# Kernel tuning notes

Measured on AMD Instinct MI355X. Metric: run time of the kernel, lower is better.

## Reference

```python
import jax, jax.numpy as jnp
import numpy as np

GROUPS = 8
EPS = 1e-5


def setup_inputs() -> dict:
    key = jax.random.key(0)
    ks = jax.random.split(key, 3)
    b, c, h, w = 8, 256, 64, 64
    return {
        "x": jax.random.normal(ks[0], (b, c, h, w), dtype=jnp.float32),
        "norm_w": jnp.ones((c,), jnp.float32),
        "norm_b": jnp.zeros((c,), jnp.float32),
        "qkv_w": jax.random.normal(ks[1], (3 * c, c), dtype=jnp.float32) * (1.0 / np.sqrt(c)),
        "qkv_b": jnp.zeros((3 * c,), jnp.float32),
        "proj_w": jax.random.normal(ks[2], (c, c), dtype=jnp.float32) * (1.0 / np.sqrt(c)),
        "proj_b": jnp.zeros((c,), jnp.float32),
    }


def _group_norm(x, w, b):
    B, C, H, W = x.shape
    xg = x.reshape(B, GROUPS, C // GROUPS, H, W)
    mean = xg.mean(axis=(2, 3, 4), keepdims=True)
    var = xg.var(axis=(2, 3, 4), keepdims=True)
    xn = ((xg - mean) * jax.lax.rsqrt(var + EPS)).reshape(B, C, H, W)
    return xn * w[None, :, None, None] + b[None, :, None, None]


def reference(x, norm_w, norm_b, qkv_w, qkv_b, proj_w, proj_b):
    B, C, H, W = x.shape
    xn = _group_norm(x, norm_w, norm_b)
    # 1x1 conv == per-pixel matmul: [B,3C,H,W]
    qkv = jnp.einsum('bchw,oc->bohw', xn, qkv_w) + qkv_b[None, :, None, None]
    q, k, v = jnp.split(qkv, 3, axis=1)  # each [B,C,H,W]
    hw = H * W
    q = q.reshape(B, C, hw).transpose(0, 2, 1)  # [B,hw,C]
    k = k.reshape(B, C, hw)                     # [B,C,hw]
    v = v.reshape(B, C, hw).transpose(0, 2, 1)  # [B,hw,C]
    scores = jnp.einsum('bnc,bcm->bnm', q, k) / jnp.sqrt(jnp.asarray(C, x.dtype))
    attn = jax.nn.softmax(scores, axis=-1)      # [B,hw,hw]
    out = jnp.einsum('bnm,bmc->bnc', attn, v)   # [B,hw,C]
    out = out.transpose(0, 2, 1).reshape(B, C, H, W)
    out = jnp.einsum('bchw,oc->bohw', out, proj_w) + proj_b[None, :, None, None]
    return x + out
```

## Files before the change

### kernel.cpp

```cpp
#include <hip/hip_runtime.h>
#include <stdint.h>

#define BATCH 8
#define CH 256
#define HW 4096
#define OC 768

typedef __bf16 bf16;
typedef __attribute__((ext_vector_type(8))) __bf16 bf16x8;
typedef __attribute__((ext_vector_type(4))) __bf16 bf16x4;
typedef __attribute__((ext_vector_type(4))) float f32x4;
typedef long fp8x8;

#define MFMA16(a, b, c) __builtin_amdgcn_mfma_f32_16x16x32_bf16(a, b, c, 0, 0, 0)
#define MFMA8(a, b, c) __builtin_amdgcn_mfma_f32_16x16x32_fp8_fp8(a, b, c, 0, 0, 0)
#define LOG2E 1.44269504088896f

static __device__ __forceinline__ void gl2lds16(const void* g, void* l) {
  __builtin_amdgcn_global_load_lds((const __attribute__((address_space(1))) void*)g,
                                   (__attribute__((address_space(3))) void*)l, 16, 0, 0);
}

static __device__ __forceinline__ int pack4fp8(float a, float b, float c, float d) {
  int t = __builtin_amdgcn_cvt_pk_fp8_f32(a, b, 0, false);
  return __builtin_amdgcn_cvt_pk_fp8_f32(c, d, t, true);
}

__global__ __launch_bounds__(256) void trans_stats(const float* __restrict__ x,
    bf16* __restrict__ xt, float* __restrict__ partial) {
  __shared__ float tile[32][33];
  __shared__ float red[8];
  int b = blockIdx.z, ct = blockIdx.y, pt = blockIdx.x;
  int p0 = pt * 32, c0 = ct * 32;
  const float* xb = x + (size_t)b * CH * HW;
  float s = 0.f, s2 = 0.f;
#pragma unroll
  for (int i = 0; i < 4; i++) {
    int c = c0 + threadIdx.y + i * 8;
    float v = xb[(size_t)c * HW + p0 + threadIdx.x];
    tile[threadIdx.y + i * 8][threadIdx.x] = v;
    s += v;
    s2 += v * v;
  }
  int tid = threadIdx.y * 32 + threadIdx.x;
  for (int off = 32; off; off >>= 1) { s += __shfl_down(s, off); s2 += __shfl_down(s2, off); }
  if ((tid & 63) == 0) { red[(tid >> 6) * 2] = s; red[(tid >> 6) * 2 + 1] = s2; }
  __syncthreads();
  if (tid == 0) {
    float* pp = partial + ((size_t)(b * 8 + ct) * 128 + pt) * 2;
    pp[0] = red[0] + red[2] + red[4] + red[6];
    pp[1] = red[1] + red[3] + red[5] + red[7];
  }
  bf16* xtb = xt + (size_t)b * HW * CH;
#pragma unroll
  for (int i = 0; i < 4; i++) {
    int p = p0 + threadIdx.y + i * 8;
    xtb[(size_t)p * CH + c0 + threadIdx.x] = (bf16)tile[threadIdx.x][threadIdx.y + i * 8];
  }
}

__global__ __launch_bounds__(128) void gn_finalize(const float* __restrict__ partial,
    const float* __restrict__ nw, const float* __restrict__ nb,
    float* __restrict__ scale, float* __restrict__ shift) {
  int bg = blockIdx.x;
  int t = threadIdx.x;
  const float* pp = partial + (size_t)bg * 128 * 2;
  float s = pp[t * 2], s2 = pp[t * 2 + 1];
  __shared__ float red[4], mm[2];
  for (int off = 32; off; off >>= 1) { s += __shfl_down(s, off); s2 += __shfl_down(s2, off); }
  if ((t & 63) == 0) { red[(t >> 6) * 2] = s; red[(t >> 6) * 2 + 1] = s2; }
  __syncthreads();
  if (t == 0) {
    float ts = red[0] + red[2], ts2 = red[1] + red[3];
    float mean = ts * (1.0f / 131072.0f);
    float var = ts2 * (1.0f / 131072.0f) - mean * mean;
    mm[0] = mean;
    mm[1] = rsqrtf(var + 1e-5f);
  }
  __syncthreads();
  if (t < 32) {
    int b = bg >> 3, g = bg & 7, c = g * 32 + t;
    float sc = nw[c] * mm[1];
    scale[b * CH + c] = sc;
    shift[b * CH + c] = nb[c] - mm[0] * sc;
  }
}

__global__ __launch_bounds__(256) void fold_qkv(const float* __restrict__ qkv_w,
    const float* __restrict__ qkv_b, const float* __restrict__ scale,
    const float* __restrict__ shift, bf16* __restrict__ wq, float* __restrict__ bq) {
  int o = blockIdx.x, b = blockIdx.y, c = threadIdx.x;
  float w = qkv_w[o * CH + c];
  wq[((size_t)b * OC + o) * CH + c] = (bf16)(w * scale[b * CH + c]);
  float part = w * shift[b * CH + c];
  __shared__ float red[4];
  for (int off = 32; off; off >>= 1) part += __shfl_down(part, off);
  if ((threadIdx.x & 63) == 0) red[threadIdx.x >> 6] = part;
  __syncthreads();
  if (threadIdx.x == 0) bq[b * OC + o] = qkv_b[o] + red[0] + red[1] + red[2] + red[3];
}

__global__ __launch_bounds__(256) void conv_projw(const float* __restrict__ w,
                                                  bf16* __restrict__ wb) {
  int i = blockIdx.x * 256 + threadIdx.x;
  wb[i] = (bf16)w[i];
}

__global__ __launch_bounds__(256) void qkv_gemm(const bf16* __restrict__ wq,
    const float* __restrict__ bq, const bf16* __restrict__ xt,
    uint8_t* __restrict__ qt, uint8_t* __restrict__ kt, uint8_t* __restrict__ vv) {
  __shared__ __align__(16) bf16 As[2][128 * 32];
  __shared__ __align__(16) bf16 Bs[2][128 * 32];
  int b = blockIdx.z, row0 = blockIdx.y * 128, col0 = blockIdx.x * 128;
  const bf16* A = wq + (size_t)b * OC * CH + (size_t)row0 * CH;
  const bf16* Bt = xt + (size_t)b * HW * CH + (size_t)col0 * CH;
  int tid = threadIdx.x, lane = tid & 63, wave = tid >> 6;
  int wm = (wave & 1) * 64, wn = (wave >> 1) * 64;
  int l15 = lane & 15, quad = lane >> 4;
  auto stage = [&](int buf, int k0) {
#pragma unroll
    for (int i = 0; i < 2; i++) {
      int idx = i * 256 + tid, r = idx >> 2, ch = idx & 3;
      gl2lds16(A + (size_t)r * CH + k0 + ch * 8, &As[buf][idx * 8]);
    }
#pragma unroll
    for (int i = 0; i < 2; i++) {
      int idx = i * 256 + tid, r = idx >> 2, ch = idx & 3;
      gl2lds16(Bt + (size_t)r * CH + k0 + ch * 8, &Bs[buf][idx * 8]);
    }
  };
  f32x4 zero = {0.f, 0.f, 0.f, 0.f};
  f32x4 acc[4][4];
#pragma unroll
  for (int i = 0; i < 4; i++)
#pragma unroll
    for (int j = 0; j < 4; j++) acc[i][j] = zero;
  stage(0, 0);
  for (int kk = 0; kk < 8; kk++) {
    int cur = kk & 1;
    __syncthreads();
    if (kk < 7) stage(1 - cur, (kk + 1) * 32);
    bf16x8 af[4], bfr[4];
#pragma unroll
    for (int i = 0; i < 4; i++) {
      af[i] = *(const bf16x8*)(&As[cur][(wm + i * 16 + l15) * 32 + quad * 8]);
      bfr[i] = *(const bf16x8*)(&Bs[cur][(wn + i * 16 + l15) * 32 + quad * 8]);
    }
#pragma unroll
    for (int i = 0; i < 4; i++)
#pragma unroll
      for (int j = 0; j < 4; j++) acc[i][j] = MFMA16(af[i], bfr[j], acc[i][j]);
  }
#pragma unroll
  for (int i = 0; i < 4; i++) {
    int o = row0 + wm + i * 16 + quad * 4;
#pragma unroll
    for (int j = 0; j < 4; j++) {
      int p = col0 + wn + j * 16 + l15;
      float v[4];
#pragma unroll
      for (int r = 0; r < 4; r++) v[r] = acc[i][j][r] + bq[b * OC + o + r];
      if (o < CH) {
        *(int*)(qt + ((size_t)b * HW + p) * CH + o) =
            pack4fp8(v[0] * LOG2E, v[1] * LOG2E, v[2] * LOG2E, v[3] * LOG2E);
      } else if (o < 2 * CH) {
        *(int*)(kt + ((size_t)b * HW + p) * CH + (o - CH)) = pack4fp8(v[0], v[1], v[2], v[3]);
      } else {
#pragma unroll
        for (int r = 0; r < 4; r++) {
          int t8 = __builtin_amdgcn_cvt_pk_fp8_f32(v[r], 0.f, 0, false);
          vv[((size_t)b * CH + (o - 2 * CH + r)) * HW + p] = (uint8_t)(t8 & 0xff);
        }
      }
    }
  }
}

__global__ __launch_bounds__(256, 2) void attn(const uint8_t* __restrict__ qt,
    const uint8_t* __restrict__ kt, const uint8_t* __restrict__ vv,
    bf16* __restrict__ opart, float* __restrict__ lstat) {
  __shared__ __align__(16) uint8_t Ks[2][32 * 256];
  __shared__ __align__(16) uint8_t Vs[2][256 * 32];
  int b = blockIdx.z, mh = blockIdx.y, q0 = blockIdx.x * 128;
  int tid = threadIdx.x, lane = tid & 63, w = tid >> 6;
  int l15 = lane & 15, quad = lane >> 4;
  int q1 = quad >> 1, qh = quad & 1;
  const uint8_t* kb_base = kt + (size_t)b * HW * CH;
  const uint8_t* vb_base = vv + (size_t)b * CH * HW;
  auto stageKV = [&](int buf, int m0) {
    const uint8_t* kb = kb_base + (size_t)m0 * CH;
#pragma unroll
    for (int i = 0; i < 2; i++) {
      int idx = i * 256 + tid, m = idx >> 4, p16 = idx & 15;
      gl2lds16(kb + m * CH + (p16 ^ (m & 7)) * 16, &Ks[buf][idx * 16]);
    }
#pragma unroll
    for (int i = 0; i < 2; i++) {
      int idx = i * 256 + tid, c = idx >> 1;
      int h2 = (idx & 1) ^ ((idx >> 3) & 1);
      gl2lds16(vb_base + (size_t)c * HW + m0 + h2 * 16, &Vs[buf][idx * 16]);
    }
  };
  fp8x8 qf[2][8];
  const uint8_t* qb = qt + ((size_t)b * HW + q0 + w * 32) * CH;
#pragma unroll
  for (int ns = 0; ns < 2; ns++)
#pragma unroll
    for (int kc = 0; kc < 8; kc++)
      qf[ns][kc] = *(const fp8x8*)(qb + (size_t)(ns * 16 + l15) * CH + kc * 32 + quad * 8);
  f32x4 zero = {0.f, 0.f, 0.f, 0.f};
  f32x4 o[2][16];
#pragma unroll
  for (int ns = 0; ns < 2; ns++)
#pragma unroll
    for (int t = 0; t < 16; t++) o[ns][t] = zero;
  float lsum[2] = {0.f, 0.f};
  int kswz = l15 & 7;
  int vswz = (l15 >> 2) & 1;
  stageKV(0, mh * 2048);
  for (int mt = 0; mt < 64; mt++) {
    int cur = mt & 1;
    __syncthreads();
    if (mt < 63) stageKV(1 - cur, mh * 2048 + (mt + 1) * 32);
    f32x4 s[2][2];
#pragma unroll
    for (int ms = 0; ms < 2; ms++)
#pragma unroll
      for (int ns = 0; ns < 2; ns++) s[ms][ns] = zero;
#pragma unroll
    for (int kc = 0; kc < 8; kc++) {
      fp8x8 kf[2];
#pragma unroll
      for (int ms = 0; ms < 2; ms++)
        kf[ms] = *(const fp8x8*)(&Ks[cur][(ms * 16 + l15) * 256 +
                                          (((kc * 2 + q1) ^ kswz) * 16) + qh * 8]);
#pragma unroll
      for (int ms = 0; ms < 2; ms++)
#pragma unroll
        for (int ns = 0; ns < 2; ns++) s[ms][ns] = MFMA8(kf[ms], qf[ns][kc], s[ms][ns]);
    }
    fp8x8 pa[2];
#pragma unroll
    for (int ns = 0; ns < 2; ns++) {
      float p0[4], p1[4];
#pragma unroll
      for (int r = 0; r < 4; r++) {
        p0[r] = exp2f(fmaf(s[0][ns][r], 0.0625f, -2.0f));
        lsum[ns] += p0[r];
      }
#pragma unroll
      for (int r = 0; r < 4; r++) {
        p1[r] = exp2f(fmaf(s[1][ns][r], 0.0625f, -2.0f));
        lsum[ns] += p1[r];
      }
      int pk0 = pack4fp8(p0[0], p0[1], p0[2], p0[3]);
      int pk1 = pack4fp8(p1[0], p1[1], p1[2], p1[3]);
      int srcLo = ((quad & 1) * 32 + l15) << 2;
      int srcHi = srcLo + 64;
      int a0 = __builtin_amdgcn_ds_bpermute(srcLo, pk0);
      int a1 = __builtin_amdgcn_ds_bpermute(srcLo, pk1);
      int b0 = __builtin_amdgcn_ds_bpermute(srcHi, pk0);
      int b1 = __builtin_amdgcn_ds_bpermute(srcHi, pk1);
      int2 pr;
      pr.x = q1 ? a1 : a0;
      pr.y = q1 ? b1 : b0;
      pa[ns] = __builtin_bit_cast(long, pr);
    }
#pragma unroll
    for (int t = 0; t < 16; t++) {
      fp8x8 vf = *(const fp8x8*)(&Vs[cur][(2 * (t * 16 + l15) + (q1 ^ vswz)) * 16 + qh * 8]);
      o[0][t] = MFMA8(vf, pa[0], o[0][t]);
      o[1][t] = MFMA8(vf, pa[1], o[1][t]);
    }
  }
  int ncol = q0 + w * 32 + l15;
#pragma unroll
  for (int ns = 0; ns < 2; ns++) {
    float lt = lsum[ns];
    lt += __shfl_xor(lt, 16);
    lt += __shfl_xor(lt, 32);
    float inv = 1.0f / lt;
    bf16* ob = opart + (size_t)(mh * BATCH + b) * CH * HW + ncol + ns * 16;
#pragma unroll
    for (int t = 0; t < 16; t++)
#pragma unroll
      for (int r = 0; r < 4; r++)
        ob[(size_t)(t * 16 + quad * 4 + r) * HW] = (bf16)(o[ns][t][r] * inv);
    if (quad == 0)
      lstat[(size_t)(mh * BATCH + b) * HW + ncol + ns * 16] = lt;
  }
}

__global__ __launch_bounds__(256) void combine_t(const bf16* __restrict__ opart,
    const float* __restrict__ lstat, bf16* __restrict__ ot) {
  __shared__ float tile[32][33];
  int b = blockIdx.z, p0 = blockIdx.x * 32, c0 = blockIdx.y * 32;
  int tx = threadIdx.x, ty = threadIdx.y;
  int p = p0 + tx;
  float l0 = lstat[(size_t)(0 * BATCH + b) * HW + p];
  float l1 = lstat[(size_t)(1 * BATCH + b) * HW + p];
  float inv = 1.0f / (l0 + l1);
  float w0 = l0 * inv, w1 = l1 * inv;
#pragma unroll
  for (int i = 0; i < 4; i++) {
    int c = c0 + ty + i * 8;
    tile[ty + i * 8][tx] =
        w0 * (float)opart[((size_t)(0 * BATCH + b) * CH + c) * HW + p] +
        w1 * (float)opart[((size_t)(1 * BATCH + b) * CH + c) * HW + p];
  }
  __syncthreads();
#pragma unroll
  for (int i = 0; i < 4; i++) {
    int pp = p0 + ty + i * 8;
    ot[((size_t)b * HW + pp) * CH + c0 + tx] = (bf16)tile[tx][ty + i * 8];
  }
}

__global__ __launch_bounds__(256) void proj_gemm(const bf16* __restrict__ pw,
    const float* __restrict__ pbias, const bf16* __restrict__ ot,
    const float* __restrict__ x, float* __restrict__ out) {
  __shared__ __align__(16) bf16 As[2][128 * 32];
  __shared__ __align__(16) bf16 Bs[2][128 * 32];
  int b = blockIdx.z, row0 = blockIdx.y * 128, col0 = blockIdx.x * 128;
  const bf16* A = pw + (size_t)row0 * CH;
  const bf16* Bt = ot + (size_t)b * HW * CH + (size_t)col0 * CH;
  int tid = threadIdx.x, lane = tid & 63, wave = tid >> 6;
  int wm = (wave & 1) * 64, wn = (wave >> 1) * 64;
  int l15 = lane & 15, quad = lane >> 4;
  auto stage = [&](int buf, int k0) {
#pragma unroll
    for (int i = 0; i < 2; i++) {
      int idx = i * 256 + tid, r = idx >> 2, ch = idx & 3;
      gl2lds16(A + (size_t)r * CH + k0 + ch * 8, &As[buf][idx * 8]);
    }
#pragma unroll
    for (int i = 0; i < 2; i++) {
      int idx = i * 256 + tid, r = idx >> 2, ch = idx & 3;
      gl2lds16(Bt + (size_t)r * CH + k0 + ch * 8, &Bs[buf][idx * 8]);
    }
  };
  f32x4 zero = {0.f, 0.f, 0.f, 0.f};
  f32x4 acc[4][4];
#pragma unroll
  for (int i = 0; i < 4; i++)
#pragma unroll
    for (int j = 0; j < 4; j++) acc[i][j] = zero;
  stage(0, 0);
  for (int kk = 0; kk < 8; kk++) {
    int cur = kk & 1;
    __syncthreads();
    if (kk < 7) stage(1 - cur, (kk + 1) * 32);
    bf16x8 af[4], bfr[4];
#pragma unroll
    for (int i = 0; i < 4; i++) {
      af[i] = *(const bf16x8*)(&As[cur][(wm + i * 16 + l15) * 32 + quad * 8]);
      bfr[i] = *(const bf16x8*)(&Bs[cur][(wn + i * 16 + l15) * 32 + quad * 8]);
    }
#pragma unroll
    for (int i = 0; i < 4; i++)
#pragma unroll
      for (int j = 0; j < 4; j++) acc[i][j] = MFMA16(af[i], bfr[j], acc[i][j]);
  }
#pragma unroll
  for (int i = 0; i < 4; i++) {
#pragma unroll
    for (int j = 0; j < 4; j++) {
      int p = col0 + wn + j * 16 + l15;
#pragma unroll
      for (int r = 0; r < 4; r++) {
        int oo = row0 + wm + i * 16 + quad * 4 + r;
        size_t off = ((size_t)b * CH + oo) * HW + p;
        out[off] = x[off] + pbias[oo] + acc[i][j][r];
      }
    }
  }
}

extern "C" void kernel_launch(void* const* d_in, const int* in_sizes, int n_in,
                              void* d_out, int out_size, void* d_ws, size_t ws_size,
                              hipStream_t stream) {
  const float* x = (const float*)d_in[0];
  const float* nw = (const float*)d_in[1];
  const float* nb = (const float*)d_in[2];
  const float* qkvw = (const float*)d_in[3];
  const float* qkvb = (const float*)d_in[4];
  const float* projw = (const float*)d_in[5];
  const float* projb = (const float*)d_in[6];
  float* out = (float*)d_out;
  char* ws = (char*)d_ws;
  float* scale = (float*)(ws + 0);
  float* shift = (float*)(ws + 8192);
  float* bq    = (float*)(ws + 16384);
  bf16* pwb    = (bf16*)(ws + 40960);
  bf16* wq     = (bf16*)(ws + 172032);
  bf16* xt     = (bf16*)(ws + 3317760);
  uint8_t* qt  = (uint8_t*)(ws + 20094976);
  uint8_t* kt  = (uint8_t*)(ws + 36872192);
  uint8_t* vv  = (uint8_t*)(ws + 53649408);
  bf16* opart  = (bf16*)(ws + 70426624);
  float* lstat = (float*)(ws + 103981056);
  float* partial = (float*)(ws + 70426624);
  bf16* ot = xt;

  trans_stats<<<dim3(128, 8, 8), dim3(32, 8), 0, stream>>>(x, xt, partial);
  gn_finalize<<<64, 128, 0, stream>>>(partial, nw, nb, scale, shift);
  fold_qkv<<<dim3(768, 8), 256, 0, stream>>>(qkvw, qkvb, scale, shift, wq, bq);
  conv_projw<<<256, 256, 0, stream>>>(projw, pwb);
  qkv_gemm<<<dim3(32, 6, 8), 256, 0, stream>>>(wq, bq, xt, qt, kt, vv);
  attn<<<dim3(32, 2, 8), 256, 0, stream>>>(qt, kt, vv, opart, lstat);
  combine_t<<<dim3(128, 8, 8), dim3(32, 8), 0, stream>>>(opart, lstat, ot);
  proj_gemm<<<dim3(32, 2, 8), 256, 0, stream>>>(pwb, projb, ot, x, out);
}
```

Baseline: 300.5 us.

## Use 512-thread attention blocks with 16 query rows per wave

The attention kernel now launches 8 waves per block instead of 4. Each wave owns 16 query columns rather than 32, which halves the per-wave Q fragments, output accumulators and softmax state. The K/V staging is split across twice as many threads, so each thread issues one load per tensor. The aim is lower register pressure and more resident waves to hide latency. In exchange, each K/V LDS tile is reused by fewer MFMAs per wave, the block carries more barrier overhead, and the launch-bounds request of 4 blocks may not fit.

```diff
diff --git a/kernel.cpp b/kernel.cpp
--- a/kernel.cpp
+++ b/kernel.cpp
@@ -176,7 +176,7 @@
   }
 }
 
-__global__ __launch_bounds__(256, 2) void attn(const uint8_t* __restrict__ qt,
+__global__ __launch_bounds__(512, 4) void attn(const uint8_t* __restrict__ qt,
     const uint8_t* __restrict__ kt, const uint8_t* __restrict__ vv,
     bf16* __restrict__ opart, float* __restrict__ lstat) {
   __shared__ __align__(16) uint8_t Ks[2][32 * 256];
@@ -189,32 +189,26 @@
   const uint8_t* vb_base = vv + (size_t)b * CH * HW;
   auto stageKV = [&](int buf, int m0) {
     const uint8_t* kb = kb_base + (size_t)m0 * CH;
-#pragma unroll
-    for (int i = 0; i < 2; i++) {
-      int idx = i * 256 + tid, m = idx >> 4, p16 = idx & 15;
+    {
+      int idx = tid, m = idx >> 4, p16 = idx & 15;
       gl2lds16(kb + m * CH + (p16 ^ (m & 7)) * 16, &Ks[buf][idx * 16]);
     }
-#pragma unroll
-    for (int i = 0; i < 2; i++) {
-      int idx = i * 256 + tid, c = idx >> 1;
+    {
+      int idx = tid, c = idx >> 1;
       int h2 = (idx & 1) ^ ((idx >> 3) & 1);
       gl2lds16(vb_base + (size_t)c * HW + m0 + h2 * 16, &Vs[buf][idx * 16]);
     }
   };
-  fp8x8 qf[2][8];
-  const uint8_t* qb = qt + ((size_t)b * HW + q0 + w * 32) * CH;
-#pragma unroll
-  for (int ns = 0; ns < 2; ns++)
-#pragma unroll
-    for (int kc = 0; kc < 8; kc++)
-      qf[ns][kc] = *(const fp8x8*)(qb + (size_t)(ns * 16 + l15) * CH + kc * 32 + quad * 8);
+  fp8x8 qf[8];
+  const uint8_t* qb = qt + ((size_t)b * HW + q0 + w * 16) * CH;
+#pragma unroll
+  for (int kc = 0; kc < 8; kc++)
+    qf[kc] = *(const fp8x8*)(qb + (size_t)l15 * CH + kc * 32 + quad * 8);
   f32x4 zero = {0.f, 0.f, 0.f, 0.f};
-  f32x4 o[2][16];
-#pragma unroll
-  for (int ns = 0; ns < 2; ns++)
-#pragma unroll
-    for (int t = 0; t < 16; t++) o[ns][t] = zero;
-  float lsum[2] = {0.f, 0.f};
+  f32x4 o[16];
+#pragma unroll
+  for (int t = 0; t < 16; t++) o[t] = zero;
+  float lsum = 0.f;
   int kswz = l15 & 7;
   int vswz = (l15 >> 2) & 1;
   stageKV(0, mh * 2048);
@@ -222,11 +216,9 @@
     int cur = mt & 1;
     __syncthreads();
     if (mt < 63) stageKV(1 - cur, mh * 2048 + (mt + 1) * 32);
-    f32x4 s[2][2];
-#pragma unroll
-    for (int ms = 0; ms < 2; ms++)
-#pragma unroll
-      for (int ns = 0; ns < 2; ns++) s[ms][ns] = zero;
+    f32x4 s[2];
+    s[0] = zero;
+    s[1] = zero;
 #pragma unroll
     for (int kc = 0; kc < 8; kc++) {
       fp8x8 kf[2];
@@ -235,60 +227,50 @@
         kf[ms] = *(const fp8x8*)(&Ks[cur][(ms * 16 + l15) * 256 +
                                           (((kc * 2 + q1) ^ kswz) * 16) + qh * 8]);
 #pragma unroll
-      for (int ms = 0; ms < 2; ms++)
-#pragma unroll
-        for (int ns = 0; ns < 2; ns++) s[ms][ns] = MFMA8(kf[ms], qf[ns][kc], s[ms][ns]);
-    }
-    fp8x8 pa[2];
-#pragma unroll
-    for (int ns = 0; ns < 2; ns++) {
-      float p0[4], p1[4];
-#pragma unroll
-      for (int r = 0; r < 4; r++) {
-        p0[r] = exp2f(fmaf(s[0][ns][r], 0.0625f, -2.0f));
-        lsum[ns] += p0[r];
-      }
-#pragma unroll
-      for (int r = 0; r < 4; r++) {
-        p1[r] = exp2f(fmaf(s[1][ns][r], 0.0625f, -2.0f));
-        lsum[ns] += p1[r];
-      }
-      int pk0 = pack4fp8(p0[0], p0[1], p0[2], p0[3]);
-      int pk1 = pack4fp8(p1[0], p1[1], p1[2], p1[3]);
-      int srcLo = ((quad & 1) * 32 + l15) << 2;
-      int srcHi = srcLo + 64;
-      int a0 = __builtin_amdgcn_ds_bpermute(srcLo, pk0);
-      int a1 = __builtin_amdgcn_ds_bpermute(srcLo, pk1);
-      int b0 = __builtin_amdgcn_ds_bpermute(srcHi, pk0);
-      int b1 = __builtin_amdgcn_ds_bpermute(srcHi, pk1);
-      int2 pr;
-      pr.x = q1 ? a1 : a0;
-      pr.y = q1 ? b1 : b0;
-      pa[ns] = __builtin_bit_cast(long, pr);
-    }
+      for (int ms = 0; ms < 2; ms++) s[ms] = MFMA8(kf[ms], qf[kc], s[ms]);
+    }
+    float p0[4], p1[4];
+#pragma unroll
+    for (int r = 0; r < 4; r++) {
+      p0[r] = exp2f(fmaf(s[0][r], 0.0625f, -2.0f));
+      lsum += p0[r];
+    }
+#pragma unroll
+    for (int r = 0; r < 4; r++) {
+      p1[r] = exp2f(fmaf(s[1][r], 0.0625f, -2.0f));
+      lsum += p1[r];
+    }
+    int pk0 = pack4fp8(p0[0], p0[1], p0[2], p0[3]);
+    int pk1 = pack4fp8(p1[0], p1[1], p1[2], p1[3]);
+    int srcLo = ((quad & 1) * 32 + l15) << 2;
+    int srcHi = srcLo + 64;
+    int a0 = __builtin_amdgcn_ds_bpermute(srcLo, pk0);
+    int a1 = __builtin_amdgcn_ds_bpermute(srcLo, pk1);
+    int b0 = __builtin_amdgcn_ds_bpermute(srcHi, pk0);
+    int b1 = __builtin_amdgcn_ds_bpermute(srcHi, pk1);
+    int2 pr;
+    pr.x = q1 ? a1 : a0;
+    pr.y = q1 ? b1 : b0;
+    fp8x8 pa = __builtin_bit_cast(long, pr);
 #pragma unroll
     for (int t = 0; t < 16; t++) {
       fp8x8 vf = *(const fp8x8*)(&Vs[cur][(2 * (t * 16 + l15) + (q1 ^ vswz)) * 16 + qh * 8]);
-      o[0][t] = MFMA8(vf, pa[0], o[0][t]);
-      o[1][t] = MFMA8(vf, pa[1], o[1][t]);
-    }
-  }
-  int ncol = q0 + w * 32 + l15;
-#pragma unroll
-  for (int ns = 0; ns < 2; ns++) {
-    float lt = lsum[ns];
-    lt += __shfl_xor(lt, 16);
-    lt += __shfl_xor(lt, 32);
-    float inv = 1.0f / lt;
-    bf16* ob = opart + (size_t)(mh * BATCH + b) * CH * HW + ncol + ns * 16;
-#pragma unroll
-    for (int t = 0; t < 16; t++)
-#pragma unroll
-      for (int r = 0; r < 4; r++)
-        ob[(size_t)(t * 16 + quad * 4 + r) * HW] = (bf16)(o[ns][t][r] * inv);
-    if (quad == 0)
-      lstat[(size_t)(mh * BATCH + b) * HW + ncol + ns * 16] = lt;
-  }
+      o[t] = MFMA8(vf, pa, o[t]);
+    }
+  }
+  int ncol = q0 + w * 16 + l15;
+  float lt = lsum;
+  lt += __shfl_xor(lt, 16);
+  lt += __shfl_xor(lt, 32);
+  float inv = 1.0f / lt;
+  bf16* ob = opart + (size_t)(mh * BATCH + b) * CH * HW + ncol;
+#pragma unroll
+  for (int t = 0; t < 16; t++)
+#pragma unroll
+    for (int r = 0; r < 4; r++)
+      ob[(size_t)(t * 16 + quad * 4 + r) * HW] = (bf16)(o[t][r] * inv);
+  if (quad == 0)
+    lstat[(size_t)(mh * BATCH + b) * HW + ncol] = lt;
 }
 
 __global__ __launch_bounds__(256) void combine_t(const bf16* __restrict__ opart,
@@ -407,7 +389,7 @@
   fold_qkv<<<dim3(768, 8), 256, 0, stream>>>(qkvw, qkvb, scale, shift, wq, bq);
   conv_projw<<<256, 256, 0, stream>>>(projw, pwb);
   qkv_gemm<<<dim3(32, 6, 8), 256, 0, stream>>>(wq, bq, xt, qt, kt, vv);
-  attn<<<dim3(32, 2, 8), 256, 0, stream>>>(qt, kt, vv, opart, lstat);
+  attn<<<dim3(32, 2, 8), 512, 0, stream>>>(qt, kt, vv, opart, lstat);
   combine_t<<<dim3(128, 8, 8), dim3(32, 8), 0, stream>>>(opart, lstat, ot);
   proj_gemm<<<dim3(32, 2, 8), 256, 0, stream>>>(pwb, projb, ot, x, out);
 }
```

Result: slower. 314.7 us (+4.7%).

## Software-pipeline attention loop to overlap QK of next tile with PV

Applied to the files above, without the earlier changes.

Restructures the attention main loop so each iteration issues the QK^T MFMAs for tile i together with the PV MFMAs for tile i-1, then computes the softmax for tile i. V gets a third LDS buffer because each V tile now lives one iteration longer. s_setprio raises wave priority around the matrix-core section. The aim is to hide the softmax and exp latency behind independent MFMA work, at the cost of extra LDS, more register pressure and a prologue/epilogue.

```diff
diff --git a/kernel.cpp b/kernel.cpp
--- a/kernel.cpp
+++ b/kernel.cpp
@@ -180,20 +180,22 @@
     const uint8_t* __restrict__ kt, const uint8_t* __restrict__ vv,
     bf16* __restrict__ opart, float* __restrict__ lstat) {
   __shared__ __align__(16) uint8_t Ks[2][32 * 256];
-  __shared__ __align__(16) uint8_t Vs[2][256 * 32];
+  __shared__ __align__(16) uint8_t Vs[3][256 * 32];
   int b = blockIdx.z, mh = blockIdx.y, q0 = blockIdx.x * 128;
   int tid = threadIdx.x, lane = tid & 63, w = tid >> 6;
   int l15 = lane & 15, quad = lane >> 4;
   int q1 = quad >> 1, qh = quad & 1;
   const uint8_t* kb_base = kt + (size_t)b * HW * CH;
   const uint8_t* vb_base = vv + (size_t)b * CH * HW;
-  auto stageKV = [&](int buf, int m0) {
+  auto stageK = [&](int buf, int m0) {
     const uint8_t* kb = kb_base + (size_t)m0 * CH;
 #pragma unroll
     for (int i = 0; i < 2; i++) {
       int idx = i * 256 + tid, m = idx >> 4, p16 = idx & 15;
       gl2lds16(kb + m * CH + (p16 ^ (m & 7)) * 16, &Ks[buf][idx * 16]);
     }
+  };
+  auto stageV = [&](int buf, int m0) {
 #pragma unroll
     for (int i = 0; i < 2; i++) {
       int idx = i * 256 + tid, c = idx >> 1;
@@ -217,29 +219,23 @@
   float lsum[2] = {0.f, 0.f};
   int kswz = l15 & 7;
   int vswz = (l15 >> 2) & 1;
-  stageKV(0, mh * 2048);
-  for (int mt = 0; mt < 64; mt++) {
-    int cur = mt & 1;
-    __syncthreads();
-    if (mt < 63) stageKV(1 - cur, mh * 2048 + (mt + 1) * 32);
-    f32x4 s[2][2];
-#pragma unroll
-    for (int ms = 0; ms < 2; ms++)
-#pragma unroll
-      for (int ns = 0; ns < 2; ns++) s[ms][ns] = zero;
+  fp8x8 pa[2];
+
+  auto qk = [&](int kbuf, f32x4 (&s)[2][2]) {
 #pragma unroll
     for (int kc = 0; kc < 8; kc++) {
       fp8x8 kf[2];
 #pragma unroll
       for (int ms = 0; ms < 2; ms++)
-        kf[ms] = *(const fp8x8*)(&Ks[cur][(ms * 16 + l15) * 256 +
-                                          (((kc * 2 + q1) ^ kswz) * 16) + qh * 8]);
+        kf[ms] = *(const fp8x8*)(&Ks[kbuf][(ms * 16 + l15) * 256 +
+                                           (((kc * 2 + q1) ^ kswz) * 16) + qh * 8]);
 #pragma unroll
       for (int ms = 0; ms < 2; ms++)
 #pragma unroll
         for (int ns = 0; ns < 2; ns++) s[ms][ns] = MFMA8(kf[ms], qf[ns][kc], s[ms][ns]);
     }
-    fp8x8 pa[2];
+  };
+  auto softmax = [&](f32x4 (&s)[2][2]) {
 #pragma unroll
     for (int ns = 0; ns < 2; ns++) {
       float p0[4], p1[4];
@@ -266,13 +262,47 @@
       pr.y = q1 ? b1 : b0;
       pa[ns] = __builtin_bit_cast(long, pr);
     }
+  };
+  auto pv = [&](int vbuf) {
 #pragma unroll
     for (int t = 0; t < 16; t++) {
-      fp8x8 vf = *(const fp8x8*)(&Vs[cur][(2 * (t * 16 + l15) + (q1 ^ vswz)) * 16 + qh * 8]);
+      fp8x8 vf = *(const fp8x8*)(&Vs[vbuf][(2 * (t * 16 + l15) + (q1 ^ vswz)) * 16 + qh * 8]);
       o[0][t] = MFMA8(vf, pa[0], o[0][t]);
       o[1][t] = MFMA8(vf, pa[1], o[1][t]);
     }
-  }
+  };
+
+  int m0base = mh * 2048;
+  stageK(0, m0base);
+  stageV(0, m0base);
+  stageK(1, m0base + 32);
+  stageV(1, m0base + 32);
+  __syncthreads();
+  {
+    f32x4 s[2][2] = {{zero, zero}, {zero, zero}};
+    qk(0, s);
+    softmax(s);
+  }
+  int vread = 0;
+  int vstage = 2;
+  for (int i = 1; i < 64; i++) {
+    int kcur = i & 1;
+    __syncthreads();
+    if (i < 63) {
+      int m0n = m0base + (i + 1) * 32;
+      stageK(1 - kcur, m0n);
+      stageV(vstage, m0n);
+      vstage = (vstage == 2) ? 0 : vstage + 1;
+    }
+    f32x4 s[2][2] = {{zero, zero}, {zero, zero}};
+    __builtin_amdgcn_s_setprio(1);
+    qk(kcur, s);
+    pv(vread);
+    __builtin_amdgcn_s_setprio(0);
+    softmax(s);
+    vread = (vread == 2) ? 0 : vread + 1;
+  }
+  pv(vread);
   int ncol = q0 + w * 32 + l15;
 #pragma unroll
   for (int ns = 0; ns < 2; ns++) {
```

Measured after the change: 292.6 us. -2.6%, faster.
